# Performance work log

Hardware: AMD Instinct MI355X
Metric: run time of the kernel (lower is better)

Reference implementation:

```python
import jax, jax.numpy as jnp
import numpy as np

IN_C = 31
OUT_C = 31
GRID = 5          # grid_size
K = 3             # spline_order
NUM_BASIS = GRID + K                  # 8 B-spline basis functions
COEF_LEN = IN_C * OUT_C * NUM_BASIS   # 7688
UW_LEN = IN_C * OUT_C                 # 961 (univariate_weight)
RW_LEN = IN_C * OUT_C                 # 961 (residual_weight)
PNUM = COEF_LEN + UW_LEN + RW_LEN     # 9610 = kan_params_num


def _ext_grid():
    # uniform grid on grid_range=(-1,1), extended by K knots on each side
    h = 2.0 / GRID
    return jnp.arange(-K, GRID + K + 1, dtype=jnp.float32) * h - 1.0  # (GRID+2K+1,)


def bspline_basis(x):
    # x: (N, IN_C) -> (N, IN_C, NUM_BASIS) via Cox-de Boor recursion
    grid = _ext_grid()
    xx = x[..., None]
    b = ((xx >= grid[:-1]) & (xx < grid[1:])).astype(x.dtype)
    for p in range(1, K + 1):
        left = (xx - grid[: -(p + 1)]) / (grid[p:-1] - grid[: -(p + 1)]) * b[..., :-1]
        right = (grid[p + 1:] - xx) / (grid[p + 1:] - grid[1:-p]) * b[..., 1:]
        b = left + right
    return b


def setup_inputs() -> dict:
    key = jax.random.key(0)
    k1, k2, k3 = jax.random.split(key, 3)
    x = jax.random.normal(k1, (1, IN_C, 128, 128), jnp.float32)
    # HyperspectralGeneratorLayer: per-pixel (1x1 conv) map in_channels -> kan_params_num
    gen_w = jax.random.normal(k2, (PNUM, IN_C), jnp.float32) * 0.02
    gen_b = jax.random.normal(k3, (PNUM,), jnp.float32) * 0.02
    return {"x": x, "gen_w": gen_w, "gen_b": gen_b}


def reference(x, gen_w, gen_b):
    B, C, H, W = x.shape
    xf = x.transpose(0, 2, 3, 1).reshape(B * H * W, C)      # (N, 31)
    # generator: per-pixel KAN parameter vector (N, 9610)
    w = xf @ gen_w.T + gen_b
    coef = w[:, :COEF_LEN].reshape(-1, IN_C, OUT_C, NUM_BASIS)
    uw = w[:, COEF_LEN:COEF_LEN + UW_LEN].reshape(-1, IN_C, OUT_C)
    rw = w[:, COEF_LEN + UW_LEN:].reshape(-1, IN_C, OUT_C)
    # per-pixel KAN: phi_ij(x_i) = uw_ij * spline_ij(x_i) + rw_ij * silu(x_i); y_j = sum_i phi_ij
    basis = bspline_basis(xf)                               # (N, 31, 8)
    spline = jnp.einsum('nik,niok->nio', basis, coef)       # (N, 31, 31)
    y = jnp.einsum('nio,nio->no', spline, uw) \
        + jnp.einsum('ni,nio->no', jax.nn.silu(xf), rw)     # (N, 31)
    return y.reshape(B, H, W, OUT_C).transpose(0, 3, 1, 2)
```

## Files before the change

kernel.cpp:

```cpp
#include <hip/hip_runtime.h>
#include <hip/hip_bf16.h>
#include <math.h>

#define IN_C 31
#define OUT_C 31
#define NPIX 16384
#define UW_OFF 7688
#define RW_OFF 8649
#define PART_OFF (640 * 1024)
#define CHUNK_BYTES 20480

typedef __attribute__((ext_vector_type(8))) _Float16 f16x8;
typedef __attribute__((ext_vector_type(4))) float f32x4;

__device__ inline short f2h(float f) {
    union { _Float16 h; short s; } cv;
    cv.h = (_Float16)f;
    return cv.s;
}

__global__ __launch_bounds__(64) void kan_prep_kernel(
    const float* __restrict__ gw, const float* __restrict__ gb,
    unsigned short* __restrict__ ws)
{
    const int blk = blockIdx.x;
    const int i   = blk / 20;
    const int ch  = blk % 20;
    const int l   = threadIdx.x;
    const int col = l & 15;
    const int krow = l >> 4;
    const int o = (ch & 1) * 16 + col;

    int p;
    if (ch < 16)      p = (i * 31 + o) * 8 + (ch >> 1);
    else if (ch < 18) p = UW_OFF + i * 31 + o;
    else              p = RW_OFF + i * 31 + o;

    short v8[8];
#pragma unroll
    for (int j = 0; j < 8; ++j) {
        const int c = krow * 8 + j;
        float v = 0.f;
        if (o < OUT_C) v = (c < IN_C) ? gw[p * 31 + c] : gb[p];
        v8[j] = f2h(v);
    }
    *(f16x8*)&ws[(blk * 64 + l) * 8] = *(f16x8*)v8;
}

__device__ __forceinline__ void stage_i(const unsigned char* wsrc,
                                        unsigned char* ldst, int t) {
#pragma unroll
    for (int k = 0; k < 2; ++k) {
        const int off = (k * 512 + t) * 16;
        __builtin_amdgcn_global_load_lds(
            (const __attribute__((address_space(1))) unsigned int*)(wsrc + off),
            (__attribute__((address_space(3))) unsigned int*)(ldst + off),
            16, 0, 0);
    }
    if (t < 256) {
        const int off = (1024 + t) * 16;
        __builtin_amdgcn_global_load_lds(
            (const __attribute__((address_space(1))) unsigned int*)(wsrc + off),
            (__attribute__((address_space(3))) unsigned int*)(ldst + off),
            16, 0, 0);
    }
}

__global__ __launch_bounds__(512) void kan_mfma13_kernel(
    const float* __restrict__ x,
    const unsigned char* __restrict__ wsw,
    float* __restrict__ parts,
    float* __restrict__ out,
    int nsplit)
{
    const int t = threadIdx.x;
    const int l = t & 63;
    const int w = t >> 6;
    const int pix0 = blockIdx.x * 256;
    const int csize = (IN_C + nsplit - 1) / nsplit;
    const int ibase = blockIdx.y * csize;
    const int ni = min(csize, IN_C - ibase);

    __shared__ __align__(16) unsigned char bufs[4][CHUNK_BYTES];

    const int n0 = w * 32;
    const int pr0 = pix0 + n0 + (l & 15);

    for (int ci = 0; ci < ni; ++ci)
        stage_i(wsw + (size_t)(ibase + ci) * CHUNK_BYTES, bufs[ci], t);

    f16x8 xv8f[2];
#pragma unroll
    for (int mt = 0; mt < 2; ++mt) {
        const int row = pr0 + mt * 16;
        const int cb = (l >> 4) * 8;
#pragma unroll
        for (int j = 0; j < 8; ++j) {
            const int c = cb + j;
            const float v = (c < IN_C) ? x[c * NPIX + row] : 1.0f;
            xv8f[mt][j] = (_Float16)v;
        }
    }

    f32x4 Y[2][2];
#pragma unroll
    for (int mt = 0; mt < 2; ++mt)
#pragma unroll
        for (int nt = 0; nt < 2; ++nt) Y[mt][nt] = (f32x4){0.f, 0.f, 0.f, 0.f};

    __syncthreads();

#pragma unroll 1
    for (int ci = 0; ci < ni; ++ci) {
        const int i = ibase + ci;
        const unsigned char* wb = bufs[ci];

        const float xa0 = x[i * NPIX + pr0];
        const float xa1 = x[i * NPIX + pr0 + 16];

        _Float16 basA[2][8];
        float silA[2];
#pragma unroll
        for (int s = 0; s < 2; ++s) {
            const float xv = (s == 0) ? xa0 : xa1;
            const float tb = (xv + 2.2f) * 2.5f;
            const float jf = floorf(tb);
            const float u  = tb - jf;
            const int  jj  = (int)jf;
            const float u2 = u * u, u3 = u2 * u;
            const float b0v = u3 * (1.f / 6.f);
            const float b1v = (-3.f * u3 + 3.f * u2 + 3.f * u + 1.f) * (1.f / 6.f);
            const float b2v = (3.f * u3 - 6.f * u2 + 4.f) * (1.f / 6.f);
            const float omu = 1.f - u;
            const float b3v = omu * omu * omu * (1.f / 6.f);
#pragma unroll
            for (int m = 0; m < 8; ++m) {
                const int d = jj - m;
                const float bv = (d == 0) ? b0v : (d == 1) ? b1v : (d == 2) ? b2v
                               : (d == 3) ? b3v : 0.f;
                basA[s][m] = (_Float16)bv;
            }
            silA[s] = xv / (1.f + __expf(-xv));
        }

        f32x4 SP[2][2];
#pragma unroll
        for (int mt = 0; mt < 2; ++mt)
#pragma unroll
            for (int nt = 0; nt < 2; ++nt) SP[mt][nt] = (f32x4){0.f, 0.f, 0.f, 0.f};

#pragma unroll
        for (int p = 0; p < 8; ++p) {
            const f16x8 b0 = *(const f16x8*)(wb + ((p * 2 + 0) * 64 + l) * 16);
            const f16x8 b1 = *(const f16x8*)(wb + ((p * 2 + 1) * 64 + l) * 16);
#pragma unroll
            for (int mt = 0; mt < 2; ++mt) {
                const f16x8 af = xv8f[mt] * basA[mt][p];
                SP[mt][0] = __builtin_amdgcn_mfma_f32_16x16x32_f16(af, b0, SP[mt][0], 0, 0, 0);
                SP[mt][1] = __builtin_amdgcn_mfma_f32_16x16x32_f16(af, b1, SP[mt][1], 0, 0, 0);
            }
        }
        {
            const f16x8 u0 = *(const f16x8*)(wb + (16 * 64 + l) * 16);
            const f16x8 u1 = *(const f16x8*)(wb + (17 * 64 + l) * 16);
            const f32x4 z = (f32x4){0.f, 0.f, 0.f, 0.f};
#pragma unroll
            for (int mt = 0; mt < 2; ++mt) {
                const f32x4 uw0 = __builtin_amdgcn_mfma_f32_16x16x32_f16(xv8f[mt], u0, z, 0, 0, 0);
                const f32x4 uw1 = __builtin_amdgcn_mfma_f32_16x16x32_f16(xv8f[mt], u1, z, 0, 0, 0);
#pragma unroll
                for (int r = 0; r < 4; ++r) {
                    Y[mt][0][r] = fmaf(uw0[r], SP[mt][0][r], Y[mt][0][r]);
                    Y[mt][1][r] = fmaf(uw1[r], SP[mt][1][r], Y[mt][1][r]);
                }
            }
        }
        {
            const f16x8 r0 = *(const f16x8*)(wb + (18 * 64 + l) * 16);
            const f16x8 r1 = *(const f16x8*)(wb + (19 * 64 + l) * 16);
#pragma unroll
            for (int mt = 0; mt < 2; ++mt) {
                const f16x8 arw = xv8f[mt] * (_Float16)silA[mt];
                Y[mt][0] = __builtin_amdgcn_mfma_f32_16x16x32_f16(arw, r0, Y[mt][0], 0, 0, 0);
                Y[mt][1] = __builtin_amdgcn_mfma_f32_16x16x32_f16(arw, r1, Y[mt][1], 0, 0, 0);
            }
        }
    }

    __syncthreads();
    float* yb = (float*)bufs;
#pragma unroll
    for (int mt = 0; mt < 2; ++mt)
#pragma unroll
        for (int nt = 0; nt < 2; ++nt)
#pragma unroll
            for (int r = 0; r < 4; ++r) {
                const int p = n0 + mt * 16 + (l >> 4) * 4 + r;
                const int o = nt * 16 + (l & 15);
                if (o < OUT_C) yb[p * 33 + o] = Y[mt][nt][r];
            }
    __syncthreads();

    float* dst = (blockIdx.y == 0) ? out
               : (parts + (size_t)(blockIdx.y - 1) * OUT_C * NPIX);
    for (int idx = t; idx < 256 * OUT_C; idx += 512) {
        const int n = idx & 255, o = idx >> 8;
        dst[o * NPIX + pix0 + n] = yb[n * 33 + o];
    }
}

__global__ __launch_bounds__(256) void kan_combine_kernel(
    float* __restrict__ out, const float* __restrict__ parts, int npart)
{
    const int e = blockIdx.x * 256 + threadIdx.x;
    const int nv = (OUT_C * NPIX) / 4;
    if (e < nv) {
        f32x4 a = ((const f32x4*)out)[e];
        for (int j = 0; j < npart; ++j)
            a += ((const f32x4*)parts)[e + (size_t)j * nv];
        ((f32x4*)out)[e] = a;
    }
}

extern "C" void kernel_launch(void* const* d_in, const int* in_sizes, int n_in,
                              void* d_out, int out_size, void* d_ws, size_t ws_size,
                              hipStream_t stream) {
    const float* x  = (const float*)d_in[0];
    const float* gw = (const float*)d_in[1];
    const float* gb = (const float*)d_in[2];
    float* out = (float*)d_out;
    unsigned short* ws = (unsigned short*)d_ws;
    float* parts = (float*)((char*)d_ws + PART_OFF);

    const size_t part_bytes = (size_t)OUT_C * NPIX * 4;
    int nsplit = 8;
    if (ws_size < PART_OFF + 7 * part_bytes) nsplit = 4;
    if (ws_size < PART_OFF + 3 * part_bytes) nsplit = 2;

    hipLaunchKernelGGL(kan_prep_kernel, dim3(620), dim3(64), 0, stream, gw, gb, ws);
    hipLaunchKernelGGL(kan_mfma13_kernel, dim3(NPIX / 256, nsplit), dim3(512), 0, stream,
                       x, (const unsigned char*)d_ws, parts, out, nsplit);
    const int nv = (OUT_C * NPIX) / 4;
    hipLaunchKernelGGL(kan_combine_kernel, dim3((nv + 255) / 256), dim3(256), 0, stream,
                       out, parts, nsplit - 1);
}
```

Baseline: 42.59 us.

## Read weights directly from global, shrink blocks, apply basis scaling in fp32

Removes LDS staging of per-input-channel weight chunks and has each wave read weight fragments directly from global memory (L2-cached). Blocks shrink from 512 threads over 256 pixels to 128 threads over 64 pixels, which raises the block count and lowers LDS use. The MFMA operands are swapped so weights are the A operand and unmodified x is the B operand, with basis values and silu applied as fp32 FMAs on the outputs instead of scaling fp16 operands. The cost is more VALU FMAs per MFMA and repeated global/L2 weight reads across many more blocks.

```diff
diff --git a/kernel.cpp b/kernel.cpp
--- a/kernel.cpp
+++ b/kernel.cpp
@@ -47,26 +47,7 @@
     *(f16x8*)&ws[(blk * 64 + l) * 8] = *(f16x8*)v8;
 }
 
-__device__ __forceinline__ void stage_i(const unsigned char* wsrc,
-                                        unsigned char* ldst, int t) {
-#pragma unroll
-    for (int k = 0; k < 2; ++k) {
-        const int off = (k * 512 + t) * 16;
-        __builtin_amdgcn_global_load_lds(
-            (const __attribute__((address_space(1))) unsigned int*)(wsrc + off),
-            (__attribute__((address_space(3))) unsigned int*)(ldst + off),
-            16, 0, 0);
-    }
-    if (t < 256) {
-        const int off = (1024 + t) * 16;
-        __builtin_amdgcn_global_load_lds(
-            (const __attribute__((address_space(1))) unsigned int*)(wsrc + off),
-            (__attribute__((address_space(3))) unsigned int*)(ldst + off),
-            16, 0, 0);
-    }
-}
-
-__global__ __launch_bounds__(512) void kan_mfma13_kernel(
+__global__ __launch_bounds__(128) void kan_mfma16_kernel(
     const float* __restrict__ x,
     const unsigned char* __restrict__ wsw,
     float* __restrict__ parts,
@@ -76,53 +57,45 @@
     const int t = threadIdx.x;
     const int l = t & 63;
     const int w = t >> 6;
-    const int pix0 = blockIdx.x * 256;
+    const int pix0 = blockIdx.x * 64;
     const int csize = (IN_C + nsplit - 1) / nsplit;
     const int ibase = blockIdx.y * csize;
-    const int ni = min(csize, IN_C - ibase);
-
-    __shared__ __align__(16) unsigned char bufs[4][CHUNK_BYTES];
-
-    const int n0 = w * 32;
-    const int pr0 = pix0 + n0 + (l & 15);
-
-    for (int ci = 0; ci < ni; ++ci)
-        stage_i(wsw + (size_t)(ibase + ci) * CHUNK_BYTES, bufs[ci], t);
-
-    f16x8 xv8f[2];
-#pragma unroll
-    for (int mt = 0; mt < 2; ++mt) {
-        const int row = pr0 + mt * 16;
+    const int iend = min(ibase + csize, IN_C);
+
+    __shared__ float yb[64 * 33];
+
+    const int pr0 = pix0 + w * 32 + (l & 15);
+
+    f16x8 ax0, ax1;
+    {
         const int cb = (l >> 4) * 8;
 #pragma unroll
         for (int j = 0; j < 8; ++j) {
             const int c = cb + j;
-            const float v = (c < IN_C) ? x[c * NPIX + row] : 1.0f;
-            xv8f[mt][j] = (_Float16)v;
+            ax0[j] = (_Float16)((c < IN_C) ? x[c * NPIX + pr0] : 1.0f);
+            ax1[j] = (_Float16)((c < IN_C) ? x[c * NPIX + pr0 + 16] : 1.0f);
         }
     }
 
     f32x4 Y[2][2];
 #pragma unroll
-    for (int mt = 0; mt < 2; ++mt)
-#pragma unroll
-        for (int nt = 0; nt < 2; ++nt) Y[mt][nt] = (f32x4){0.f, 0.f, 0.f, 0.f};
-
-    __syncthreads();
+    for (int ot = 0; ot < 2; ++ot)
+#pragma unroll
+        for (int pt = 0; pt < 2; ++pt) Y[ot][pt] = (f32x4){0.f, 0.f, 0.f, 0.f};
+
+    const f32x4 z = (f32x4){0.f, 0.f, 0.f, 0.f};
 
 #pragma unroll 1
-    for (int ci = 0; ci < ni; ++ci) {
-        const int i = ibase + ci;
-        const unsigned char* wb = bufs[ci];
-
-        const float xa0 = x[i * NPIX + pr0];
-        const float xa1 = x[i * NPIX + pr0 + 16];
-
-        _Float16 basA[2][8];
-        float silA[2];
+    for (int i = ibase; i < iend; ++i) {
+        const f16x8* wg = (const f16x8*)(wsw + (size_t)i * CHUNK_BYTES);
+
+        const float xv0 = x[i * NPIX + pr0];
+        const float xv1 = x[i * NPIX + pr0 + 16];
+
+        float bas0[8], bas1[8], sil0, sil1;
 #pragma unroll
         for (int s = 0; s < 2; ++s) {
-            const float xv = (s == 0) ? xa0 : xa1;
+            const float xv = (s == 0) ? xv0 : xv1;
             const float tb = (xv + 2.2f) * 2.5f;
             const float jf = floorf(tb);
             const float u  = tb - jf;
@@ -138,73 +111,72 @@
                 const int d = jj - m;
                 const float bv = (d == 0) ? b0v : (d == 1) ? b1v : (d == 2) ? b2v
                                : (d == 3) ? b3v : 0.f;
-                basA[s][m] = (_Float16)bv;
-            }
-            silA[s] = xv / (1.f + __expf(-xv));
+                if (s == 0) bas0[m] = bv; else bas1[m] = bv;
+            }
+            const float sv = xv / (1.f + __expf(-xv));
+            if (s == 0) sil0 = sv; else sil1 = sv;
         }
 
         f32x4 SP[2][2];
 #pragma unroll
-        for (int mt = 0; mt < 2; ++mt)
-#pragma unroll
-            for (int nt = 0; nt < 2; ++nt) SP[mt][nt] = (f32x4){0.f, 0.f, 0.f, 0.f};
+        for (int ot = 0; ot < 2; ++ot)
+#pragma unroll
+            for (int pt = 0; pt < 2; ++pt) SP[ot][pt] = z;
 
 #pragma unroll
         for (int p = 0; p < 8; ++p) {
-            const f16x8 b0 = *(const f16x8*)(wb + ((p * 2 + 0) * 64 + l) * 16);
-            const f16x8 b1 = *(const f16x8*)(wb + ((p * 2 + 1) * 64 + l) * 16);
-#pragma unroll
-            for (int mt = 0; mt < 2; ++mt) {
-                const f16x8 af = xv8f[mt] * basA[mt][p];
-                SP[mt][0] = __builtin_amdgcn_mfma_f32_16x16x32_f16(af, b0, SP[mt][0], 0, 0, 0);
-                SP[mt][1] = __builtin_amdgcn_mfma_f32_16x16x32_f16(af, b1, SP[mt][1], 0, 0, 0);
+            const f16x8 a0 = wg[(p * 2 + 0) * 64 + l];
+            const f16x8 a1 = wg[(p * 2 + 1) * 64 + l];
+            const f32x4 T00 = __builtin_amdgcn_mfma_f32_16x16x32_f16(a0, ax0, z, 0, 0, 0);
+            const f32x4 T01 = __builtin_amdgcn_mfma_f32_16x16x32_f16(a0, ax1, z, 0, 0, 0);
+            const f32x4 T10 = __builtin_amdgcn_mfma_f32_16x16x32_f16(a1, ax0, z, 0, 0, 0);
+            const f32x4 T11 = __builtin_amdgcn_mfma_f32_16x16x32_f16(a1, ax1, z, 0, 0, 0);
+#pragma unroll
+            for (int r = 0; r < 4; ++r) {
+                SP[0][0][r] = fmaf(bas0[p], T00[r], SP[0][0][r]);
+                SP[0][1][r] = fmaf(bas1[p], T01[r], SP[0][1][r]);
+                SP[1][0][r] = fmaf(bas0[p], T10[r], SP[1][0][r]);
+                SP[1][1][r] = fmaf(bas1[p], T11[r], SP[1][1][r]);
             }
         }
         {
-            const f16x8 u0 = *(const f16x8*)(wb + (16 * 64 + l) * 16);
-            const f16x8 u1 = *(const f16x8*)(wb + (17 * 64 + l) * 16);
-            const f32x4 z = (f32x4){0.f, 0.f, 0.f, 0.f};
-#pragma unroll
-            for (int mt = 0; mt < 2; ++mt) {
-                const f32x4 uw0 = __builtin_amdgcn_mfma_f32_16x16x32_f16(xv8f[mt], u0, z, 0, 0, 0);
-                const f32x4 uw1 = __builtin_amdgcn_mfma_f32_16x16x32_f16(xv8f[mt], u1, z, 0, 0, 0);
+            const f16x8 u0 = wg[16 * 64 + l];
+            const f16x8 u1 = wg[17 * 64 + l];
+            const f16x8 r0 = wg[18 * 64 + l];
+            const f16x8 r1 = wg[19 * 64 + l];
+#pragma unroll
+            for (int pt = 0; pt < 2; ++pt) {
+                const f16x8 axp = (pt == 0) ? ax0 : ax1;
+                const float sil = (pt == 0) ? sil0 : sil1;
+                const f32x4 UW0 = __builtin_amdgcn_mfma_f32_16x16x32_f16(u0, axp, z, 0, 0, 0);
+                const f32x4 UW1 = __builtin_amdgcn_mfma_f32_16x16x32_f16(u1, axp, z, 0, 0, 0);
+                const f32x4 R0  = __builtin_amdgcn_mfma_f32_16x16x32_f16(r0, axp, z, 0, 0, 0);
+                const f32x4 R1  = __builtin_amdgcn_mfma_f32_16x16x32_f16(r1, axp, z, 0, 0, 0);
 #pragma unroll
                 for (int r = 0; r < 4; ++r) {
-                    Y[mt][0][r] = fmaf(uw0[r], SP[mt][0][r], Y[mt][0][r]);
-                    Y[mt][1][r] = fmaf(uw1[r], SP[mt][1][r], Y[mt][1][r]);
+                    Y[0][pt][r] = fmaf(UW0[r], SP[0][pt][r], fmaf(sil, R0[r], Y[0][pt][r]));
+                    Y[1][pt][r] = fmaf(UW1[r], SP[1][pt][r], fmaf(sil, R1[r], Y[1][pt][r]));
                 }
             }
         }
-        {
-            const f16x8 r0 = *(const f16x8*)(wb + (18 * 64 + l) * 16);
-            const f16x8 r1 = *(const f16x8*)(wb + (19 * 64 + l) * 16);
-#pragma unroll
-            for (int mt = 0; mt < 2; ++mt) {
-                const f16x8 arw = xv8f[mt] * (_Float16)silA[mt];
-                Y[mt][0] = __builtin_amdgcn_mfma_f32_16x16x32_f16(arw, r0, Y[mt][0], 0, 0, 0);
-                Y[mt][1] = __builtin_amdgcn_mfma_f32_16x16x32_f16(arw, r1, Y[mt][1], 0, 0, 0);
-            }
-        }
-    }
-
-    __syncthreads();
-    float* yb = (float*)bufs;
-#pragma unroll
-    for (int mt = 0; mt < 2; ++mt)
-#pragma unroll
-        for (int nt = 0; nt < 2; ++nt)
+    }
+
+#pragma unroll
+    for (int ot = 0; ot < 2; ++ot)
+#pragma unroll
+        for (int pt = 0; pt < 2; ++pt)
 #pragma unroll
             for (int r = 0; r < 4; ++r) {
-                const int p = n0 + mt * 16 + (l >> 4) * 4 + r;
-                const int o = nt * 16 + (l & 15);
-                if (o < OUT_C) yb[p * 33 + o] = Y[mt][nt][r];
+                const int o = ot * 16 + (l >> 4) * 4 + r;
+                const int p = w * 32 + pt * 16 + (l & 15);
+                if (o < OUT_C) yb[p * 33 + o] = Y[ot][pt][r];
             }
     __syncthreads();
 
     float* dst = (blockIdx.y == 0) ? out
                : (parts + (size_t)(blockIdx.y - 1) * OUT_C * NPIX);
-    for (int idx = t; idx < 256 * OUT_C; idx += 512) {
-        const int n = idx & 255, o = idx >> 8;
+    for (int idx = t; idx < 64 * OUT_C; idx += 128) {
+        const int n = idx & 63, o = idx >> 6;
         dst[o * NPIX + pix0 + n] = yb[n * 33 + o];
     }
 }
@@ -238,7 +210,7 @@
     if (ws_size < PART_OFF + 3 * part_bytes) nsplit = 2;
 
     hipLaunchKernelGGL(kan_prep_kernel, dim3(620), dim3(64), 0, stream, gw, gb, ws);
-    hipLaunchKernelGGL(kan_mfma13_kernel, dim3(NPIX / 256, nsplit), dim3(512), 0, stream,
+    hipLaunchKernelGGL(kan_mfma16_kernel, dim3(NPIX / 64, nsplit), dim3(128), 0, stream,
                        x, (const unsigned char*)d_ws, parts, out, nsplit);
     const int nv = (OUT_C * NPIX) / 4;
     hipLaunchKernelGGL(kan_combine_kernel, dim3((nv + 255) / 256), dim3(256), 0, stream,
```

Result: slower. 56.92 us (+33.6%).
